# Optimization experiments

Measured on AMD Instinct MI355X. Metric: run time of the kernel, lower is better.

## Reference

```python
import jax, jax.numpy as jnp
import numpy as np

B, T, ADIM = 64, 2048, 384
NUM_EMB, HID_DIM = 10, 3


def setup_inputs() -> dict:
    key = jax.random.key(0)
    ks = jax.random.split(key, 9)
    return {
        "hs_ref_embs": jax.random.normal(ks[0], (B, T, ADIM), dtype=jnp.float32),
        "inds": jax.random.randint(ks[1], (B, T), 0, NUM_EMB, dtype=jnp.int64),
        "codebook": jax.random.normal(ks[2], (NUM_EMB, HID_DIM), dtype=jnp.float32),
        "W_ih": jax.random.normal(ks[3], (4 * NUM_EMB, ADIM), dtype=jnp.float32) * 0.05,
        "W_hh": jax.random.normal(ks[4], (4 * NUM_EMB, NUM_EMB), dtype=jnp.float32) * 0.05,
        "b_ih": jax.random.normal(ks[5], (4 * NUM_EMB,), dtype=jnp.float32) * 0.05,
        "b_hh": jax.random.normal(ks[6], (4 * NUM_EMB,), dtype=jnp.float32) * 0.05,
        "qs_W": jax.random.normal(ks[7], (ADIM, HID_DIM), dtype=jnp.float32) * 0.05,
        "qs_b": jax.random.normal(ks[8], (ADIM,), dtype=jnp.float32) * 0.05,
    }


def _lstm_cell(x, h, c, W_ih, W_hh, b_ih, b_hh):
    # PyTorch LSTMCell: gates = x @ W_ih^T + b_ih + h @ W_hh^T + b_hh
    gates = x @ W_ih.T + b_ih + h @ W_hh.T + b_hh  # (B, 4H)
    i, f, g, o = jnp.split(gates, 4, axis=-1)
    i, f, o = jax.nn.sigmoid(i), jax.nn.sigmoid(f), jax.nn.sigmoid(o)
    g = jnp.tanh(g)
    c_new = f * c + i * g
    h_new = o * jnp.tanh(c_new)
    return h_new, c_new


def reference(hs_ref_embs, inds, codebook, W_ih, W_hh, b_ih, b_hh, qs_W, qs_b):
    Bsz, Tmax, _ = hs_ref_embs.shape
    H = codebook.shape[0]  # num_embeddings (= LSTM hidden size)
    D = codebook.shape[1]  # hidden_dim

    def step(carry, xs):
        h, c, prev_emb = carry
        x_t, is_first = xs
        qs = prev_emb @ qs_W.T + qs_b  # (B, adim)
        inp = jnp.where(is_first, x_t, x_t + qs)
        h, c = _lstm_cell(inp, h, c, W_ih, W_hh, b_ih, b_hh)
        scores = jax.nn.log_softmax(h, axis=-1)  # (B, H)
        top_ind = jnp.argmax(scores, axis=-1)    # top-1, indices not differentiated
        emb = codebook[top_ind]                  # (B, D) gather == one-hot matmul
        return (h, c, emb), (scores, emb)

    init = (
        jnp.zeros((Bsz, H), hs_ref_embs.dtype),
        jnp.zeros((Bsz, H), hs_ref_embs.dtype),
        jnp.zeros((Bsz, D), hs_ref_embs.dtype),
    )
    xs = (jnp.swapaxes(hs_ref_embs, 0, 1), jnp.arange(Tmax) == 0)
    _, (scores, embs) = jax.lax.scan(step, init, xs)
    scores = jnp.swapaxes(scores, 0, 1)  # (B, T, H) log-probs
    embs = jnp.swapaxes(embs, 0, 1)      # (B, T, D)
    # NLLLoss(mean): -mean over (B,T) of log-prob at ground-truth index
    picked = jnp.take_along_axis(scores, inds[..., None], axis=-1)[..., 0]
    loss = -jnp.mean(picked)
    return embs, loss
```

## Files before the change

### kernel.cpp

```cpp
#include <hip/hip_runtime.h>
#include <math.h>

#define BB 64
#define TT 2048
#define ADIM 384
#define NE 10
#define NG 40
#define HD 3

#define OFF_X32   0ULL
#define OFF_ETAB  (41943040ULL + 122880ULL)
#define OFF_BIAS0 (OFF_ETAB + 3200ULL)
#define OFF_H     (OFF_BIAS0 + 320ULL)
#define OFF_IDX   (OFF_H + 5242880ULL)
#define OFF_PART  (OFF_IDX + 524288ULL)
#define OFF_DUMP  (OFF_PART + 4096ULL)

__device__ __forceinline__ float fexp2(float x) {
    float r;
    asm("v_exp_f32 %0, %1" : "=v"(r) : "v"(x));
    return r;
}
__device__ __forceinline__ float frcp(float d) {
    float r;
    asm("v_rcp_f32 %0, %1" : "=v"(r) : "v"(d));
    return r;
}

template<int CTRL>
__device__ __forceinline__ float dpp_mov_f32(float x) {
    int v = __float_as_int(x);
    v = __builtin_amdgcn_update_dpp(v, v, CTRL, 0xF, 0xF, true);
    return __int_as_float(v);
}
template<int CTRL, int RMASK>
__device__ __forceinline__ unsigned dpp_mov_u32(unsigned x) {
    int v = __builtin_amdgcn_update_dpp((int)x, (int)x, CTRL, RMASK, 0xF, true);
    return (unsigned)v;
}
__device__ __forceinline__ unsigned umax2(unsigned a, unsigned b) {
    return a > b ? a : b;
}

__global__ __launch_bounds__(64) void setup_kernel(
        const float* __restrict__ W_ih, const float* __restrict__ codebook,
        const float* __restrict__ qs_W, const float* __restrict__ qs_b,
        const float* __restrict__ b_ih, const float* __restrict__ b_hh,
        float* __restrict__ EtabB, float* __restrict__ BIAS0) {
    int k = threadIdx.x;
    if (k >= NG) return;
    double M0 = 0, M1 = 0, M2 = 0, qb = 0;
    for (int a = 0; a < ADIM; ++a) {
        double w = (double)W_ih[k * ADIM + a];
        M0 = fma(w, (double)qs_W[a * HD + 0], M0);
        M1 = fma(w, (double)qs_W[a * HD + 1], M1);
        M2 = fma(w, (double)qs_W[a * HD + 2], M2);
        qb = fma(w, (double)qs_b[a], qb);
    }
    double bias = (double)b_ih[k] + (double)b_hh[k];
    for (int i = 0; i < NE; ++i) {
        double e = bias + qb;
        e = fma((double)codebook[i * HD + 0], M0, e);
        e = fma((double)codebook[i * HD + 1], M1, e);
        e = fma((double)codebook[i * HD + 2], M2, e);
        EtabB[i * NG + k] = (float)e;
    }
    BIAS0[k] = (float)bias;
}

__global__ __launch_bounds__(256) void gemm_kernel(
        const float* __restrict__ hs, const float* __restrict__ W_ih,
        float* __restrict__ X32) {
    int lane = threadIdx.x & 63;
    int wv = threadIdx.x >> 6;
    int cb = __builtin_amdgcn_readfirstlane(wv * 10);
    long row = (long)blockIdx.x * 64 + lane;
    const float* xr = hs + row * ADIM;
    float accA[10], accB[10];
#pragma unroll
    for (int j = 0; j < 10; ++j) { accA[j] = 0.0f; accB[j] = 0.0f; }
    for (int a0 = 0; a0 < ADIM; a0 += 4) {
        float4 xv = *(const float4*)(xr + a0);
#pragma unroll
        for (int j = 0; j < 10; ++j) {
            float4 wv4 = *(const float4*)(W_ih + (cb + j) * ADIM + a0);
            accA[j] = fmaf(wv4.x, xv.x, accA[j]);
            accA[j] = fmaf(wv4.y, xv.y, accA[j]);
            accB[j] = fmaf(wv4.z, xv.z, accB[j]);
            accB[j] = fmaf(wv4.w, xv.w, accB[j]);
        }
    }
    float* op = X32 + row * NG + cb;
#pragma unroll
    for (int j = 0; j < 10; ++j) op[j] = accA[j] + accB[j];
}

__global__ __launch_bounds__(64) void recur_kernel(
        const float* __restrict__ X32,
        const float* __restrict__ W_hh, const float* __restrict__ EtabB,
        const float* __restrict__ BIAS0, char* __restrict__ ws) {
    const int k = threadIdx.x;
    const int b = blockIdx.x;
    const int j = k & 3;
    const int m = k >> 2;
    const bool valid = (k < NG);
    const int col = valid ? (j * 10 + m) : (NG - 1);
    const bool isg = (j == 2);

    const float LOG2E = 1.44269504088896340736f;
    const float Lg   = isg ? (-2.0f * LOG2E) : (-LOG2E);
    const float amul = isg ? 2.0f : 1.0f;
    const float aadd = isg ? -1.0f : 0.0f;
    const float L2   = -2.0f * LOG2E;

    float whh[NE];
#pragma unroll
    for (int mm = 0; mm < NE; ++mm) whh[mm] = W_hh[col * NE + mm];
    float etab[NE];
#pragma unroll
    for (int i = 0; i < NE; ++i) etab[i] = EtabB[i * NG + col];

    const float* Xb = X32 + (long)b * TT * NG;

    const bool is_h = ((k & 3) == 0) && valid;
    const bool is_i = (k == NG);
    unsigned voff = is_h ? (unsigned)(OFF_H + ((unsigned)b * TT * NE + m) * 4u)
                  : is_i ? (unsigned)(OFF_IDX + (unsigned)b * TT * 4u)
                         : (unsigned)OFF_DUMP;
    const unsigned vstep = is_h ? (unsigned)(NE * 4) : is_i ? 4u : 0u;

    const unsigned vmask = valid ? 0xFFFFFFFFu : 0u;

    float xs0 = Xb[0 * NG + col];
    float xs1 = Xb[1 * NG + col];
    float xs2 = Xb[2 * NG + col];
    float xs3 = Xb[3 * NG + col];

    float ha[NE];
#pragma unroll
    for (int mm = 0; mm < NE; ++mm) ha[mm] = 0.0f;
    float c = 0.0f;
    float esel = BIAS0[col];

    auto step = [&](float& xslot, int t) {
        float xg = xslot;
        xslot = Xb[(t + 4) * NG + col];

        float p0 = fmaf(ha[1], whh[1], ha[0] * whh[0]);
        float p1 = fmaf(ha[3], whh[3], ha[2] * whh[2]);
        float p2 = fmaf(ha[5], whh[5], ha[4] * whh[4]);
        float p3 = fmaf(ha[7], whh[7], ha[6] * whh[6]);
        float p4 = fmaf(ha[9], whh[9], ha[8] * whh[8]);
        float dotE = ((p0 + p1) + (p2 + p3)) + (p4 + esel);
        float g32 = xg + dotE;

        float e1 = fexp2(g32 * Lg);
        float r1 = frcp(1.0f + e1);
        float act = fmaf(amul, r1, aadd);

        float fiv = dpp_mov_f32<0x00>(act);
        float ffv = dpp_mov_f32<0x55>(act);
        float fgv = dpp_mov_f32<0xAA>(act);
        float fov = dpp_mov_f32<0xFF>(act);
        c = fmaf(ffv, c, fiv * fgv);

        float e2 = fexp2(fabsf(c) * L2);
        float r2 = frcp(1.0f + e2);
        float th = fmaf(2.0f, r2, -1.0f);
        float habs = fov * th;
        int hI = __float_as_int(habs) | (__float_as_int(c) & 0x80000000);

        int smsk = hI >> 31;
        unsigned key0 = ((unsigned)(hI ^ (smsk | (int)0x80000000))) & vmask;
        unsigned kr = umax2(key0, dpp_mov_u32<0x124, 0xF>(key0));
        kr = umax2(kr, dpp_mov_u32<0x128, 0xF>(kr));
        kr = umax2(kr, dpp_mov_u32<0x142, 0xA>(kr));
        kr = umax2(kr, dpp_mov_u32<0x143, 0xC>(kr));
        unsigned sMax = (unsigned)__builtin_amdgcn_readlane((int)kr, 32);
        unsigned long long ball = __ballot(key0 == sMax);
        int s_idx = ((int)__builtin_ctzll(ball)) >> 2;

        int val = is_h ? hI : s_idx;
        *(int*)(ws + voff) = val;
        voff += vstep;

#pragma unroll
        for (int mm = 0; mm < NE; ++mm)
            ha[mm] = __int_as_float(__builtin_amdgcn_readlane(hI, 4 * mm));

        float a0 = (s_idx & 1) ? etab[1] : etab[0];
        float a1 = (s_idx & 1) ? etab[3] : etab[2];
        float a2 = (s_idx & 1) ? etab[5] : etab[4];
        float a3 = (s_idx & 1) ? etab[7] : etab[6];
        float a4 = (s_idx & 1) ? etab[9] : etab[8];
        float b0 = (s_idx & 2) ? a1 : a0;
        float b1 = (s_idx & 2) ? a3 : a2;
        float c0 = (s_idx & 4) ? b1 : b0;
        esel = (s_idx & 8) ? a4 : c0;
    };

    for (int t = 0; t < TT; t += 4) {
        step(xs0, t);
        step(xs1, t + 1);
        step(xs2, t + 2);
        step(xs3, t + 3);
    }
}

__global__ __launch_bounds__(256) void tail_kernel(
        const float* __restrict__ h_ws, const int* __restrict__ idx_ws,
        const int* __restrict__ inds, const float* __restrict__ codebook,
        float* __restrict__ out_embs, double* __restrict__ partials) {
    int i = blockIdx.x * 256 + threadIdx.x;
    int idx = idx_ws[i];
    out_embs[i * 3 + 0] = codebook[idx * 3 + 0];
    out_embs[i * 3 + 1] = codebook[idx * 3 + 1];
    out_embs[i * 3 + 2] = codebook[idx * 3 + 2];

    const float* hp = h_ws + (long)i * NE;
    double hv[NE];
#pragma unroll
    for (int mm = 0; mm < NE; ++mm) hv[mm] = (double)hp[mm];
    double mx = hv[0];
#pragma unroll
    for (int mm = 1; mm < NE; ++mm) mx = fmax(mx, hv[mm]);
    double sdn = 0.0;
#pragma unroll
    for (int mm = 0; mm < NE; ++mm) sdn += exp(hv[mm] - mx);
    int ind = inds[i];
    double picked = (double)hp[ind] - (mx + log(sdn));

    __shared__ double red[256];
    red[threadIdx.x] = picked;
    __syncthreads();
    for (int st = 128; st > 0; st >>= 1) {
        if (threadIdx.x < st) red[threadIdx.x] += red[threadIdx.x + st];
        __syncthreads();
    }
    if (threadIdx.x == 0) partials[blockIdx.x] = red[0];
}

__global__ __launch_bounds__(256) void final_kernel(
        const double* __restrict__ partials, float* __restrict__ out_loss) {
    __shared__ double red[256];
    red[threadIdx.x] = partials[threadIdx.x] + partials[threadIdx.x + 256];
    __syncthreads();
    for (int st = 128; st > 0; st >>= 1) {
        if (threadIdx.x < st) red[threadIdx.x] += red[threadIdx.x + st];
        __syncthreads();
    }
    if (threadIdx.x == 0)
        out_loss[0] = (float)(-red[0] / (double)(BB * TT));
}

extern "C" void kernel_launch(void* const* d_in, const int* in_sizes, int n_in,
                              void* d_out, int out_size, void* d_ws, size_t ws_size,
                              hipStream_t stream) {
    const float* hs       = (const float*)d_in[0];
    const int*   inds     = (const int*)d_in[1];
    const float* codebook = (const float*)d_in[2];
    const float* W_ih     = (const float*)d_in[3];
    const float* W_hh     = (const float*)d_in[4];
    const float* b_ih     = (const float*)d_in[5];
    const float* b_hh     = (const float*)d_in[6];
    const float* qs_W     = (const float*)d_in[7];
    const float* qs_b     = (const float*)d_in[8];
    float* out = (float*)d_out;

    char* ws = (char*)d_ws;
    float*  X32   = (float*)(ws + OFF_X32);
    float*  EtabB = (float*)(ws + OFF_ETAB);
    float*  BIAS0 = (float*)(ws + OFF_BIAS0);
    float*  h_ws  = (float*)(ws + OFF_H);
    int*    idx_ws= (int*)(ws + OFF_IDX);
    double* part  = (double*)(ws + OFF_PART);

    setup_kernel<<<1, 64, 0, stream>>>(W_ih, codebook, qs_W, qs_b, b_ih, b_hh,
                                       EtabB, BIAS0);
    gemm_kernel<<<2048, 256, 0, stream>>>(hs, W_ih, X32);
    recur_kernel<<<BB, 64, 0, stream>>>(X32, W_hh, EtabB, BIAS0, ws);
    tail_kernel<<<512, 256, 0, stream>>>(h_ws, idx_ws, inds, codebook, out, part);
    final_kernel<<<1, 256, 0, stream>>>(part, out + (size_t)BB * TT * HD);
}
```

Baseline: 570.2 us.

## Fuse setup, GEMM, recurrence and tail into one persistent kernel with flag sync

Merges the setup, input-projection GEMM, per-batch LSTM recurrence and the loss/embedding tail into a single launch. Recurrence blocks spin on per-batch bitmask flags set by the GEMM blocks, so each batch's sequential scan can begin once its first time chunks of projected input exist, overlapping the GEMM with the serial recurrence. The tail work is done by the same block right after its scan, and the final reduction shrinks to 64 partials. It relies on recurrence blocks 0-64 being resident before the GEMM blocks that feed them, and adds spin-wait polling and a memset.

```diff
diff --git a/kernel.cpp b/kernel.cpp
--- a/kernel.cpp
+++ b/kernel.cpp
@@ -15,6 +15,7 @@
 #define OFF_IDX   (OFF_H + 5242880ULL)
 #define OFF_PART  (OFF_IDX + 524288ULL)
 #define OFF_DUMP  (OFF_PART + 4096ULL)
+#define OFF_SYNC  (OFF_DUMP + 256ULL)
 
 __device__ __forceinline__ float fexp2(float x) {
     float r;
@@ -41,216 +42,254 @@
 __device__ __forceinline__ unsigned umax2(unsigned a, unsigned b) {
     return a > b ? a : b;
 }
-
-__global__ __launch_bounds__(64) void setup_kernel(
-        const float* __restrict__ W_ih, const float* __restrict__ codebook,
-        const float* __restrict__ qs_W, const float* __restrict__ qs_b,
-        const float* __restrict__ b_ih, const float* __restrict__ b_hh,
-        float* __restrict__ EtabB, float* __restrict__ BIAS0) {
-    int k = threadIdx.x;
-    if (k >= NG) return;
-    double M0 = 0, M1 = 0, M2 = 0, qb = 0;
-    for (int a = 0; a < ADIM; ++a) {
-        double w = (double)W_ih[k * ADIM + a];
-        M0 = fma(w, (double)qs_W[a * HD + 0], M0);
-        M1 = fma(w, (double)qs_W[a * HD + 1], M1);
-        M2 = fma(w, (double)qs_W[a * HD + 2], M2);
-        qb = fma(w, (double)qs_b[a], qb);
-    }
-    double bias = (double)b_ih[k] + (double)b_hh[k];
-    for (int i = 0; i < NE; ++i) {
-        double e = bias + qb;
-        e = fma((double)codebook[i * HD + 0], M0, e);
-        e = fma((double)codebook[i * HD + 1], M1, e);
-        e = fma((double)codebook[i * HD + 2], M2, e);
-        EtabB[i * NG + k] = (float)e;
-    }
-    BIAS0[k] = (float)bias;
-}
-
-__global__ __launch_bounds__(256) void gemm_kernel(
+__device__ __forceinline__ unsigned aload(const unsigned* p) {
+    return __hip_atomic_load(p, __ATOMIC_ACQUIRE, __HIP_MEMORY_SCOPE_AGENT);
+}
+__device__ __forceinline__ void spin_prefix(const unsigned* mp, int c_hi) {
+    for (;;) {
+        unsigned inv = ~aload(mp);
+        int lowest = inv ? (__ffs(inv) - 1) : 32;
+        if (lowest > c_hi) return;
+        __builtin_amdgcn_s_sleep(4);
+    }
+}
+
+__global__ __launch_bounds__(256) void mega_kernel(
         const float* __restrict__ hs, const float* __restrict__ W_ih,
-        float* __restrict__ X32) {
-    int lane = threadIdx.x & 63;
-    int wv = threadIdx.x >> 6;
-    int cb = __builtin_amdgcn_readfirstlane(wv * 10);
-    long row = (long)blockIdx.x * 64 + lane;
-    const float* xr = hs + row * ADIM;
-    float accA[10], accB[10];
-#pragma unroll
-    for (int j = 0; j < 10; ++j) { accA[j] = 0.0f; accB[j] = 0.0f; }
-    for (int a0 = 0; a0 < ADIM; a0 += 4) {
-        float4 xv = *(const float4*)(xr + a0);
-#pragma unroll
-        for (int j = 0; j < 10; ++j) {
-            float4 wv4 = *(const float4*)(W_ih + (cb + j) * ADIM + a0);
-            accA[j] = fmaf(wv4.x, xv.x, accA[j]);
-            accA[j] = fmaf(wv4.y, xv.y, accA[j]);
-            accB[j] = fmaf(wv4.z, xv.z, accB[j]);
-            accB[j] = fmaf(wv4.w, xv.w, accB[j]);
-        }
-    }
-    float* op = X32 + row * NG + cb;
-#pragma unroll
-    for (int j = 0; j < 10; ++j) op[j] = accA[j] + accB[j];
-}
-
-__global__ __launch_bounds__(64) void recur_kernel(
-        const float* __restrict__ X32,
-        const float* __restrict__ W_hh, const float* __restrict__ EtabB,
-        const float* __restrict__ BIAS0, char* __restrict__ ws) {
-    const int k = threadIdx.x;
-    const int b = blockIdx.x;
-    const int j = k & 3;
-    const int m = k >> 2;
-    const bool valid = (k < NG);
-    const int col = valid ? (j * 10 + m) : (NG - 1);
-    const bool isg = (j == 2);
-
-    const float LOG2E = 1.44269504088896340736f;
-    const float Lg   = isg ? (-2.0f * LOG2E) : (-LOG2E);
-    const float amul = isg ? 2.0f : 1.0f;
-    const float aadd = isg ? -1.0f : 0.0f;
-    const float L2   = -2.0f * LOG2E;
-
-    float whh[NE];
-#pragma unroll
-    for (int mm = 0; mm < NE; ++mm) whh[mm] = W_hh[col * NE + mm];
-    float etab[NE];
-#pragma unroll
-    for (int i = 0; i < NE; ++i) etab[i] = EtabB[i * NG + col];
-
-    const float* Xb = X32 + (long)b * TT * NG;
-
-    const bool is_h = ((k & 3) == 0) && valid;
-    const bool is_i = (k == NG);
-    unsigned voff = is_h ? (unsigned)(OFF_H + ((unsigned)b * TT * NE + m) * 4u)
-                  : is_i ? (unsigned)(OFF_IDX + (unsigned)b * TT * 4u)
-                         : (unsigned)OFF_DUMP;
-    const unsigned vstep = is_h ? (unsigned)(NE * 4) : is_i ? 4u : 0u;
-
-    const unsigned vmask = valid ? 0xFFFFFFFFu : 0u;
-
-    float xs0 = Xb[0 * NG + col];
-    float xs1 = Xb[1 * NG + col];
-    float xs2 = Xb[2 * NG + col];
-    float xs3 = Xb[3 * NG + col];
-
-    float ha[NE];
-#pragma unroll
-    for (int mm = 0; mm < NE; ++mm) ha[mm] = 0.0f;
-    float c = 0.0f;
-    float esel = BIAS0[col];
-
-    auto step = [&](float& xslot, int t) {
-        float xg = xslot;
-        xslot = Xb[(t + 4) * NG + col];
-
-        float p0 = fmaf(ha[1], whh[1], ha[0] * whh[0]);
-        float p1 = fmaf(ha[3], whh[3], ha[2] * whh[2]);
-        float p2 = fmaf(ha[5], whh[5], ha[4] * whh[4]);
-        float p3 = fmaf(ha[7], whh[7], ha[6] * whh[6]);
-        float p4 = fmaf(ha[9], whh[9], ha[8] * whh[8]);
-        float dotE = ((p0 + p1) + (p2 + p3)) + (p4 + esel);
-        float g32 = xg + dotE;
-
-        float e1 = fexp2(g32 * Lg);
-        float r1 = frcp(1.0f + e1);
-        float act = fmaf(amul, r1, aadd);
-
-        float fiv = dpp_mov_f32<0x00>(act);
-        float ffv = dpp_mov_f32<0x55>(act);
-        float fgv = dpp_mov_f32<0xAA>(act);
-        float fov = dpp_mov_f32<0xFF>(act);
-        c = fmaf(ffv, c, fiv * fgv);
-
-        float e2 = fexp2(fabsf(c) * L2);
-        float r2 = frcp(1.0f + e2);
-        float th = fmaf(2.0f, r2, -1.0f);
-        float habs = fov * th;
-        int hI = __float_as_int(habs) | (__float_as_int(c) & 0x80000000);
-
-        int smsk = hI >> 31;
-        unsigned key0 = ((unsigned)(hI ^ (smsk | (int)0x80000000))) & vmask;
-        unsigned kr = umax2(key0, dpp_mov_u32<0x124, 0xF>(key0));
-        kr = umax2(kr, dpp_mov_u32<0x128, 0xF>(kr));
-        kr = umax2(kr, dpp_mov_u32<0x142, 0xA>(kr));
-        kr = umax2(kr, dpp_mov_u32<0x143, 0xC>(kr));
-        unsigned sMax = (unsigned)__builtin_amdgcn_readlane((int)kr, 32);
-        unsigned long long ball = __ballot(key0 == sMax);
-        int s_idx = ((int)__builtin_ctzll(ball)) >> 2;
-
-        int val = is_h ? hI : s_idx;
-        *(int*)(ws + voff) = val;
-        voff += vstep;
-
-#pragma unroll
-        for (int mm = 0; mm < NE; ++mm)
-            ha[mm] = __int_as_float(__builtin_amdgcn_readlane(hI, 4 * mm));
-
-        float a0 = (s_idx & 1) ? etab[1] : etab[0];
-        float a1 = (s_idx & 1) ? etab[3] : etab[2];
-        float a2 = (s_idx & 1) ? etab[5] : etab[4];
-        float a3 = (s_idx & 1) ? etab[7] : etab[6];
-        float a4 = (s_idx & 1) ? etab[9] : etab[8];
-        float b0 = (s_idx & 2) ? a1 : a0;
-        float b1 = (s_idx & 2) ? a3 : a2;
-        float c0 = (s_idx & 4) ? b1 : b0;
-        esel = (s_idx & 8) ? a4 : c0;
-    };
-
-    for (int t = 0; t < TT; t += 4) {
-        step(xs0, t);
-        step(xs1, t + 1);
-        step(xs2, t + 2);
-        step(xs3, t + 3);
-    }
-}
-
-__global__ __launch_bounds__(256) void tail_kernel(
-        const float* __restrict__ h_ws, const int* __restrict__ idx_ws,
-        const int* __restrict__ inds, const float* __restrict__ codebook,
-        float* __restrict__ out_embs, double* __restrict__ partials) {
-    int i = blockIdx.x * 256 + threadIdx.x;
-    int idx = idx_ws[i];
-    out_embs[i * 3 + 0] = codebook[idx * 3 + 0];
-    out_embs[i * 3 + 1] = codebook[idx * 3 + 1];
-    out_embs[i * 3 + 2] = codebook[idx * 3 + 2];
-
-    const float* hp = h_ws + (long)i * NE;
-    double hv[NE];
-#pragma unroll
-    for (int mm = 0; mm < NE; ++mm) hv[mm] = (double)hp[mm];
-    double mx = hv[0];
-#pragma unroll
-    for (int mm = 1; mm < NE; ++mm) mx = fmax(mx, hv[mm]);
-    double sdn = 0.0;
-#pragma unroll
-    for (int mm = 0; mm < NE; ++mm) sdn += exp(hv[mm] - mx);
-    int ind = inds[i];
-    double picked = (double)hp[ind] - (mx + log(sdn));
-
+        const float* __restrict__ codebook, const float* __restrict__ qs_W,
+        const float* __restrict__ qs_b, const float* __restrict__ b_ih,
+        const float* __restrict__ b_hh, const float* __restrict__ W_hh,
+        const int* __restrict__ inds, float* __restrict__ out_embs,
+        char* __restrict__ ws) {
+    unsigned* sync = (unsigned*)(ws + OFF_SYNC);
+    float* X32 = (float*)(ws + OFF_X32);
+    const int blk = blockIdx.x;
+
+    if (blk >= 65) {
+        int gblk = blk - 65;
+        int lane = threadIdx.x & 63;
+        int wv = threadIdx.x >> 6;
+        int cb = __builtin_amdgcn_readfirstlane(wv * 10);
+        long row = (long)gblk * 64 + lane;
+        const float* xr = hs + row * ADIM;
+        float accA[10], accB[10];
+#pragma unroll
+        for (int j = 0; j < 10; ++j) { accA[j] = 0.0f; accB[j] = 0.0f; }
+        for (int a0 = 0; a0 < ADIM; a0 += 4) {
+            float4 xv = *(const float4*)(xr + a0);
+#pragma unroll
+            for (int j = 0; j < 10; ++j) {
+                float4 wv4 = *(const float4*)(W_ih + (cb + j) * ADIM + a0);
+                accA[j] = fmaf(wv4.x, xv.x, accA[j]);
+                accA[j] = fmaf(wv4.y, xv.y, accA[j]);
+                accB[j] = fmaf(wv4.z, xv.z, accB[j]);
+                accB[j] = fmaf(wv4.w, xv.w, accB[j]);
+            }
+        }
+        float* op = X32 + row * NG + cb;
+#pragma unroll
+        for (int j = 0; j < 10; ++j) op[j] = accA[j] + accB[j];
+        __syncthreads();
+        if (threadIdx.x == 0) {
+            __threadfence();
+            __hip_atomic_fetch_or(&sync[1 + (gblk >> 5)], 1u << (gblk & 31),
+                                  __ATOMIC_RELEASE, __HIP_MEMORY_SCOPE_AGENT);
+        }
+        return;
+    }
+
+    if (blk == 64) {
+        float* EtabB = (float*)(ws + OFF_ETAB);
+        float* BIAS0 = (float*)(ws + OFF_BIAS0);
+        int k = threadIdx.x;
+        if (k < NG) {
+            double M0 = 0, M1 = 0, M2 = 0, qb = 0;
+            for (int a = 0; a < ADIM; ++a) {
+                double w = (double)W_ih[k * ADIM + a];
+                M0 = fma(w, (double)qs_W[a * HD + 0], M0);
+                M1 = fma(w, (double)qs_W[a * HD + 1], M1);
+                M2 = fma(w, (double)qs_W[a * HD + 2], M2);
+                qb = fma(w, (double)qs_b[a], qb);
+            }
+            double bias = (double)b_ih[k] + (double)b_hh[k];
+            for (int i = 0; i < NE; ++i) {
+                double e = bias + qb;
+                e = fma((double)codebook[i * HD + 0], M0, e);
+                e = fma((double)codebook[i * HD + 1], M1, e);
+                e = fma((double)codebook[i * HD + 2], M2, e);
+                EtabB[i * NG + k] = (float)e;
+            }
+            BIAS0[k] = (float)bias;
+        }
+        __syncthreads();
+        if (threadIdx.x == 0) {
+            __threadfence();
+            __hip_atomic_store(&sync[0], 1u, __ATOMIC_RELEASE,
+                               __HIP_MEMORY_SCOPE_AGENT);
+        }
+        return;
+    }
+
+    const int b = blk;
+    if (threadIdx.x < 64) {
+        const int k = threadIdx.x;
+        const int j = k & 3;
+        const int m = k >> 2;
+        const bool valid = (k < NG);
+        const int col = valid ? (j * 10 + m) : (NG - 1);
+        const bool isg = (j == 2);
+
+        const float LOG2E = 1.44269504088896340736f;
+        const float Lg   = isg ? (-2.0f * LOG2E) : (-LOG2E);
+        const float amul = isg ? 2.0f : 1.0f;
+        const float aadd = isg ? -1.0f : 0.0f;
+        const float L2   = -2.0f * LOG2E;
+
+        while (aload(&sync[0]) == 0) __builtin_amdgcn_s_sleep(4);
+        spin_prefix(&sync[1 + b], 1);
+
+        const float* EtabB = (const float*)(ws + OFF_ETAB);
+        const float* BIAS0 = (const float*)(ws + OFF_BIAS0);
+        float whh[NE];
+#pragma unroll
+        for (int mm = 0; mm < NE; ++mm) whh[mm] = W_hh[col * NE + mm];
+        float etab[NE];
+#pragma unroll
+        for (int i = 0; i < NE; ++i) etab[i] = EtabB[i * NG + col];
+
+        const float* Xb = X32 + (long)b * TT * NG;
+
+        const bool is_h = ((k & 3) == 0) && valid;
+        const bool is_i = (k == NG);
+        unsigned voff = is_h ? (unsigned)(OFF_H + ((unsigned)b * TT * NE + m) * 4u)
+                      : is_i ? (unsigned)(OFF_IDX + (unsigned)b * TT * 4u)
+                             : (unsigned)OFF_DUMP;
+        const unsigned vstep = is_h ? (unsigned)(NE * 4) : is_i ? 4u : 0u;
+        const unsigned vmask = valid ? 0xFFFFFFFFu : 0u;
+
+        float xs0 = Xb[0 * NG + col];
+        float xs1 = Xb[1 * NG + col];
+        float xs2 = Xb[2 * NG + col];
+        float xs3 = Xb[3 * NG + col];
+
+        float ha[NE];
+#pragma unroll
+        for (int mm = 0; mm < NE; ++mm) ha[mm] = 0.0f;
+        float c = 0.0f;
+        float esel = BIAS0[col];
+
+        auto step = [&](float& xslot, int t) {
+            float xg = xslot;
+            xslot = Xb[(t + 4) * NG + col];
+
+            float p0 = fmaf(ha[1], whh[1], ha[0] * whh[0]);
+            float p1 = fmaf(ha[3], whh[3], ha[2] * whh[2]);
+            float p2 = fmaf(ha[5], whh[5], ha[4] * whh[4]);
+            float p3 = fmaf(ha[7], whh[7], ha[6] * whh[6]);
+            float p4 = fmaf(ha[9], whh[9], ha[8] * whh[8]);
+            float dotE = ((p0 + p1) + (p2 + p3)) + (p4 + esel);
+            float g32 = xg + dotE;
+
+            float e1 = fexp2(g32 * Lg);
+            float r1 = frcp(1.0f + e1);
+            float act = fmaf(amul, r1, aadd);
+
+            float fiv = dpp_mov_f32<0x00>(act);
+            float ffv = dpp_mov_f32<0x55>(act);
+            float fgv = dpp_mov_f32<0xAA>(act);
+            float fov = dpp_mov_f32<0xFF>(act);
+            c = fmaf(ffv, c, fiv * fgv);
+
+            float e2 = fexp2(fabsf(c) * L2);
+            float r2 = frcp(1.0f + e2);
+            float th = fmaf(2.0f, r2, -1.0f);
+            float habs = fov * th;
+            int hI = __float_as_int(habs) | (__float_as_int(c) & 0x80000000);
+
+            int smsk = hI >> 31;
+            unsigned key0 = ((unsigned)(hI ^ (smsk | (int)0x80000000))) & vmask;
+            unsigned kr = umax2(key0, dpp_mov_u32<0x124, 0xF>(key0));
+            kr = umax2(kr, dpp_mov_u32<0x128, 0xF>(kr));
+            kr = umax2(kr, dpp_mov_u32<0x142, 0xA>(kr));
+            kr = umax2(kr, dpp_mov_u32<0x143, 0xC>(kr));
+            unsigned sMax = (unsigned)__builtin_amdgcn_readlane((int)kr, 32);
+            unsigned long long ball = __ballot(key0 == sMax);
+            int s_idx = ((int)__builtin_ctzll(ball)) >> 2;
+
+            int val = is_h ? hI : s_idx;
+            *(int*)(ws + voff) = val;
+            voff += vstep;
+
+#pragma unroll
+            for (int mm = 0; mm < NE; ++mm)
+                ha[mm] = __int_as_float(__builtin_amdgcn_readlane(hI, 4 * mm));
+
+            float a0 = (s_idx & 1) ? etab[1] : etab[0];
+            float a1 = (s_idx & 1) ? etab[3] : etab[2];
+            float a2 = (s_idx & 1) ? etab[5] : etab[4];
+            float a3 = (s_idx & 1) ? etab[7] : etab[6];
+            float a4 = (s_idx & 1) ? etab[9] : etab[8];
+            float b0 = (s_idx & 2) ? a1 : a0;
+            float b1 = (s_idx & 2) ? a3 : a2;
+            float c0 = (s_idx & 4) ? b1 : b0;
+            esel = (s_idx & 8) ? a4 : c0;
+        };
+
+        for (int t = 0; t < TT; t += 4) {
+            if ((t & 63) == 0) {
+                int c_hi = (t >> 6) + 1;
+                if (c_hi > 31) c_hi = 31;
+                spin_prefix(&sync[1 + b], c_hi);
+            }
+            step(xs0, t);
+            step(xs1, t + 1);
+            step(xs2, t + 2);
+            step(xs3, t + 3);
+        }
+    }
+
+    __syncthreads();
+
+    const float* h_ws = (const float*)(ws + OFF_H);
+    const int* idx_ws = (const int*)(ws + OFF_IDX);
+    double psum = 0.0;
+    for (int t = threadIdx.x; t < TT; t += 256) {
+        long i = (long)b * TT + t;
+        int idx = idx_ws[i];
+        out_embs[i * 3 + 0] = codebook[idx * 3 + 0];
+        out_embs[i * 3 + 1] = codebook[idx * 3 + 1];
+        out_embs[i * 3 + 2] = codebook[idx * 3 + 2];
+
+        const float* hp = h_ws + i * NE;
+        double hv[NE];
+#pragma unroll
+        for (int mm = 0; mm < NE; ++mm) hv[mm] = (double)hp[mm];
+        double mx = hv[0];
+#pragma unroll
+        for (int mm = 1; mm < NE; ++mm) mx = fmax(mx, hv[mm]);
+        double sdn = 0.0;
+#pragma unroll
+        for (int mm = 0; mm < NE; ++mm) sdn += exp(hv[mm] - mx);
+        int ind = inds[i];
+        psum += (double)hp[ind] - (mx + log(sdn));
+    }
     __shared__ double red[256];
-    red[threadIdx.x] = picked;
+    red[threadIdx.x] = psum;
     __syncthreads();
     for (int st = 128; st > 0; st >>= 1) {
         if (threadIdx.x < st) red[threadIdx.x] += red[threadIdx.x + st];
         __syncthreads();
     }
-    if (threadIdx.x == 0) partials[blockIdx.x] = red[0];
-}
-
-__global__ __launch_bounds__(256) void final_kernel(
+    if (threadIdx.x == 0) ((double*)(ws + OFF_PART))[b] = red[0];
+}
+
+__global__ __launch_bounds__(64) void final_kernel(
         const double* __restrict__ partials, float* __restrict__ out_loss) {
-    __shared__ double red[256];
-    red[threadIdx.x] = partials[threadIdx.x] + partials[threadIdx.x + 256];
-    __syncthreads();
-    for (int st = 128; st > 0; st >>= 1) {
-        if (threadIdx.x < st) red[threadIdx.x] += red[threadIdx.x + st];
-        __syncthreads();
-    }
-    if (threadIdx.x == 0)
-        out_loss[0] = (float)(-red[0] / (double)(BB * TT));
+    if (threadIdx.x == 0) {
+        double s = 0.0;
+        for (int i = 0; i < BB; ++i) s += partials[i];
+        out_loss[0] = (float)(-s / (double)(BB * TT));
+    }
 }
 
 extern "C" void kernel_launch(void* const* d_in, const int* in_sizes, int n_in,
@@ -268,17 +307,10 @@
     float* out = (float*)d_out;
 
     char* ws = (char*)d_ws;
-    float*  X32   = (float*)(ws + OFF_X32);
-    float*  EtabB = (float*)(ws + OFF_ETAB);
-    float*  BIAS0 = (float*)(ws + OFF_BIAS0);
-    float*  h_ws  = (float*)(ws + OFF_H);
-    int*    idx_ws= (int*)(ws + OFF_IDX);
-    double* part  = (double*)(ws + OFF_PART);
-
-    setup_kernel<<<1, 64, 0, stream>>>(W_ih, codebook, qs_W, qs_b, b_ih, b_hh,
-                                       EtabB, BIAS0);
-    gemm_kernel<<<2048, 256, 0, stream>>>(hs, W_ih, X32);
-    recur_kernel<<<BB, 64, 0, stream>>>(X32, W_hh, EtabB, BIAS0, ws);
-    tail_kernel<<<512, 256, 0, stream>>>(h_ws, idx_ws, inds, codebook, out, part);
-    final_kernel<<<1, 256, 0, stream>>>(part, out + (size_t)BB * TT * HD);
-}
+    double* part = (double*)(ws + OFF_PART);
+
+    hipMemsetAsync(ws + OFF_SYNC, 0, 512, stream);
+    mega_kernel<<<2113, 256, 0, stream>>>(hs, W_ih, codebook, qs_W, qs_b,
+                                          b_ih, b_hh, W_hh, inds, out, ws);
+    final_kernel<<<1, 64, 0, stream>>>(part, out + (size_t)BB * TT * HD);
+}
```

New measurement: 722.1 us. 26.6% more time.
